# Kernel tuning notes

Hardware: AMD Instinct MI355X
Metric: run time of the kernel (lower is better)

Reference implementation:

```python
import jax, jax.numpy as jnp
import numpy as np

B, S, D, H, MB = 2, 2048, 2048, 32, 16
HD = D // H          # 64
N = S // MB          # 128 mini-batches
EPS = 1e-5
BASE_LR = 1.0


def setup_inputs() -> dict:
    ks = jax.random.split(jax.random.key(0), 8)
    sc = 1.0 / np.sqrt(D)
    inv = 1.0 / (10000.0 ** (np.arange(0, HD, 2, dtype=np.float64) / HD))
    return {
        "x": jax.random.normal(ks[0], (B, S, D), jnp.float32),
        "pos_frequencies": jnp.asarray(np.outer(np.arange(S), inv), jnp.float32),  # (S, HD//2) rope angles
        "Wq": jax.random.normal(ks[1], (D, D), jnp.float32) * sc,
        "Wk": jax.random.normal(ks[2], (D, D), jnp.float32) * sc,
        "Wv": jax.random.normal(ks[3], (D, D), jnp.float32) * sc,
        "Wo": jax.random.normal(ks[4], (D, D), jnp.float32) * sc,
        "post_gamma": jnp.ones((D,), jnp.float32),
        "post_beta": jnp.zeros((D,), jnp.float32),
        "ilr_W": jax.random.normal(ks[5], (H, 1, D), jnp.float32) * 0.02,  # inner_loop_lr_W
        "ilr_b": jnp.zeros((H, 1), jnp.float32),                            # inner_loop_lr_b
        "lgs": jnp.zeros((MB,), jnp.float32),                               # learnable_gradient_scale
        "ttt_gamma": jnp.ones((H, HD), jnp.float32),                        # ttt_norm_weight
        "ttt_beta": jnp.zeros((H, HD), jnp.float32),                        # ttt_norm_bias
        "W0": jax.random.normal(ks[6], (H, HD, HD), jnp.float32) / np.sqrt(HD),
        "b0": jnp.zeros((H, 1, HD), jnp.float32),
    }


def _rope(x, freqs):
    # x: (B,H,S,HD), freqs: (S,HD//2); rotate interleaved pairs
    cos = jnp.cos(freqs)[None, None]
    sin = jnp.sin(freqs)[None, None]
    x1, x2 = x[..., 0::2], x[..., 1::2]
    return jnp.stack([x1 * cos - x2 * sin, x1 * sin + x2 * cos], -1).reshape(x.shape)


def _ln_fwd(z, g, b):
    mu = z.mean(-1, keepdims=True)
    var = z.var(-1, keepdims=True)
    return g * (z - mu) * jax.lax.rsqrt(var + EPS) + b


def _ln_l2_bwd(z, tgt, g, b):
    # grad of 0.5*||LN(z) - tgt||^2 w.r.t. z (fused LayerNorm backward)
    mu = z.mean(-1, keepdims=True)
    var = z.var(-1, keepdims=True)
    rstd = jax.lax.rsqrt(var + EPS)
    zh = (z - mu) * rstd
    dy = (g * zh + b) - tgt
    dzh = dy * g
    return (dzh - dzh.mean(-1, keepdims=True) - zh * (dzh * zh).mean(-1, keepdims=True)) * rstd


def reference(x, pos_frequencies, Wq, Wk, Wv, Wo, post_gamma, post_beta,
              ilr_W, ilr_b, lgs, ttt_gamma, ttt_beta, W0, b0):
    # projections (torch Linear: x @ W.T), shape (B,H,S,HD)
    q = (x @ Wq.T).reshape(B, S, H, HD).transpose(0, 2, 1, 3)
    k = (x @ Wk.T).reshape(B, S, H, HD).transpose(0, 2, 1, 3)
    v = (x @ Wv.T).reshape(B, S, H, HD).transpose(0, 2, 1, 3)
    q = _rope(q, pos_frequencies)
    k = _rope(k, pos_frequencies)
    v = _rope(v, pos_frequencies)  # module applies RoPE to V too

    # inner-loop learning rates: (B,H,N,1,MB), gradient_scale: (MB,1)
    xr = x.reshape(B, N, MB, D)
    lr = jnp.einsum('bnkd,hod->bhnko', xr, ilr_W) + ilr_b.reshape(1, H, 1, 1, 1)
    lr = BASE_LR * jax.nn.sigmoid(lr).transpose(0, 1, 2, 4, 3) / HD
    gs = jnp.clip(1.0 / jnp.arange(1, MB + 1, dtype=jnp.float32) + lgs, 0.0)
    eta = gs.reshape(1, 1, 1, MB, 1) * lr  # (B,H,N,MB,MB)

    to_n = lambda t: t.reshape(B, H, N, MB, -1).transpose(2, 0, 1, 3, 4)
    Qn, Kn, Vn = to_n(q), to_n(k), to_n(v)           # (N,B,H,MB,HD)
    En = eta.transpose(2, 0, 1, 3, 4)                # (N,B,H,MB,MB)

    g = ttt_gamma.reshape(1, H, 1, HD)
    be = ttt_beta.reshape(1, H, 1, HD)
    W_init = jnp.broadcast_to(W0[None], (B, H, HD, HD))
    b_init = jnp.broadcast_to(b0[None], (B, H, 1, HD))

    def step(carry, inp):
        W, bb = carry
        XQ, XK, XV, E = inp
        Z = XK @ W + bb
        grad = _ln_l2_bwd(Z, XV - XK, g, be)                 # (B,H,MB,HD)
        Attn = jnp.tril(XQ @ XK.swapaxes(-1, -2))            # causal dual form
        b_bar = bb - jnp.tril(E) @ grad
        Z_bar = XQ @ W - (E * Attn) @ grad + b_bar
        last_eta = E[..., -1, :, None]                       # (B,H,MB,1)
        W_new = W - jnp.swapaxes(last_eta * XK, -1, -2) @ grad
        b_new = bb - jnp.sum(last_eta * grad, axis=-2, keepdims=True)
        return (W_new, b_new), XQ + _ln_fwd(Z_bar, g, be)

    _, ys = jax.lax.scan(step, (W_init, b_init), (Qn, Kn, Vn, En))  # ys: (N,B,H,MB,HD)
    out = ys.transpose(1, 0, 3, 2, 4).reshape(B, S, D)

    mu = out.mean(-1, keepdims=True)
    var = out.var(-1, keepdims=True)
    out = post_gamma * (out - mu) * jax.lax.rsqrt(var + EPS) + post_beta
    return out @ Wo.T
```

## Files before the change

kernel.cpp:

```cpp
#include <hip/hip_runtime.h>
#include <hip/hip_bf16.h>
#include <math.h>

#define BB 2
#define SS 2048
#define DD 2048
#define HH 32
#define HDD 64
#define MBB 16
#define NN 128

typedef unsigned short u16;
typedef short bf16x8_t __attribute__((ext_vector_type(8)));
typedef float f32x4_t __attribute__((ext_vector_type(4)));

__device__ __forceinline__ float b2f(u16 u) { return __uint_as_float(((unsigned)u) << 16); }
__device__ __forceinline__ u16 f2b(float f) {
    unsigned u = __float_as_uint(f);
    return (u16)((u + 0x7FFFu + ((u >> 16) & 1u)) >> 16);
}
__device__ __forceinline__ unsigned pk2(float a, float b) {
    return (unsigned)f2b(a) | ((unsigned)f2b(b) << 16);
}
__device__ __forceinline__ unsigned pk2r(u16 a, u16 b) { return (unsigned)a | ((unsigned)b << 16); }
__device__ __forceinline__ float wsum(float x) {
    x += __shfl_xor(x, 32);
    x += __shfl_xor(x, 16);
    x += __shfl_xor(x, 8);
    x += __shfl_xor(x, 4);
    x += __shfl_xor(x, 2);
    x += __shfl_xor(x, 1);
    return x;
}

typedef __attribute__((address_space(3))) unsigned int lds_u32;
typedef __attribute__((address_space(1))) const unsigned int glb_u32;
__device__ __forceinline__ void async_copy16(const void* g, void* l) {
    __builtin_amdgcn_global_load_lds((glb_u32*)g, (lds_u32*)l, 16, 0, 0);
}


__global__ __launch_bounds__(256) void k_cvt5(const float* __restrict__ x, const float* __restrict__ wq,
                                              const float* __restrict__ wk, const float* __restrict__ wv,
                                              const float* __restrict__ wo, u16* __restrict__ xb,
                                              u16* __restrict__ wqb, u16* __restrict__ wkb,
                                              u16* __restrict__ wvb, u16* __restrict__ wob) {
    int sl = blockIdx.y;
    long e = (long)(blockIdx.x * 256 + threadIdx.x) * 4;
    if (sl == 5) {
        long n = e >> 11;
        int cin = (int)(e & 2047);
        int hd0 = (cin >> 6) * 64 + ((cin & 63) >> 2);
        const float* src = wo + n * 2048 + hd0;
        float f0 = src[0], f1 = src[16], f2 = src[32], f3 = src[48];
        uint2 o;
        o.x = pk2(f0, f1);
        o.y = pk2(f2, f3);
        *(uint2*)(wob + e) = o;
        return;
    }
    const float* s;
    u16* d;
    if (sl == 0) { s = x; d = xb; }
    else if (sl == 1) { s = x + 4194304; d = xb + 4194304; }
    else if (sl == 2) { s = wq; d = wqb; }
    else if (sl == 3) { s = wk; d = wkb; }
    else { s = wv; d = wvb; }
    float4 f = *(const float4*)(s + e);
    uint2 o;
    o.x = pk2(f.x, f.y);
    o.y = pk2(f.z, f.w);
    *(uint2*)(d + e) = o;
}

__global__ void k_trig(const float* __restrict__ pf, float* __restrict__ ct, float* __restrict__ st) {
    int i = blockIdx.x * 256 + threadIdx.x;
    float f = pf[i];
    ct[i] = cosf(f);
    st[i] = sinf(f);
}

__global__ void k_ppg(const float* __restrict__ pg, const float* __restrict__ pb,
                      float* __restrict__ pgp, float* __restrict__ pbp) {
    int i = blockIdx.x * 256 + threadIdx.x;
    int h = i >> 6, o = i & 63;
    int src = h * 64 + (o >> 2) + (o & 3) * 16;
    pgp[i] = pg[src];
    pbp[i] = pb[src];
}

__global__ __launch_bounds__(256) void k_prep(const u16* __restrict__ qb, const u16* __restrict__ kb,
                                              u16* __restrict__ qc, u16* __restrict__ kc) {
    long row = (long)blockIdx.x * 256 + threadIdx.x;
    const u16* src = (blockIdx.y == 0 ? qb : kb) + row * 64;
    u16* dst = (blockIdx.y == 0 ? qc : kc) + row * 64;
    u16 v[64];
#pragma unroll
    for (int i = 0; i < 8; ++i) *(uint4*)&v[i * 8] = *(const uint4*)(src + i * 8);
    u16 o[64];
#pragma unroll
    for (int d = 0; d < 64; ++d) o[(d & 15) * 4 + (d >> 4)] = v[d];
#pragma unroll
    for (int i = 0; i < 8; ++i) *(uint4*)(dst + i * 8) = *(uint4*)&o[i * 8];
}

template <int EPI>
__global__ __launch_bounds__(256) void k_gemm_bt(const u16* __restrict__ A, const u16* __restrict__ B0,
                                                 const u16* __restrict__ B1, const u16* __restrict__ B2,
                                                 void* __restrict__ C0, void* __restrict__ C1,
                                                 void* __restrict__ C2, int M, int Nn, int K,
                                                 const float* __restrict__ ct, const float* __restrict__ st) {
    __shared__ u16 As[128 * 32];
    __shared__ u16 Bs[128 * 32];
    int z = blockIdx.z;
    const u16* Bm = (z == 0) ? B0 : (z == 1) ? B1 : B2;
    void* Cout = (z == 0) ? C0 : (z == 1) ? C1 : C2;
    int tid = threadIdx.x, lane = tid & 63, wv = tid >> 6;
    int m0 = blockIdx.y * 128, n0 = blockIdx.x * 128;
    int wm = wv >> 1, wn = wv & 1;

    f32x4_t acc[4][4];
    f32x4_t zero = {0.f, 0.f, 0.f, 0.f};
#pragma unroll
    for (int a = 0; a < 4; ++a)
#pragma unroll
        for (int b = 0; b < 4; ++b) acc[a][b] = zero;

    int mrow = lane & 15, qk = (lane >> 4) * 8;
    const int kTiles = K >> 5;
    for (int kt = 0; kt < kTiles; ++kt) {
        __syncthreads();
        int kb = kt << 5;
#pragma unroll
        for (int it = 0; it < 2; ++it) {
            int cb = it * 256 + wv * 64;
            int c = cb + lane;
            const u16* gpA = A + (m0 + (c >> 2)) * K + kb + ((c & 3) << 3);
            async_copy16(gpA, &As[cb << 3]);
            const u16* gpB = Bm + (n0 + (c >> 2)) * K + kb + ((c & 3) << 3);
            async_copy16(gpB, &Bs[cb << 3]);
        }
        asm volatile("s_waitcnt vmcnt(0)" ::: "memory");
        __syncthreads();

        bf16x8_t af[4], bfr[4];
#pragma unroll
        for (int mi = 0; mi < 4; ++mi)
            af[mi] = *(const bf16x8_t*)&As[(wm * 64 + mi * 16 + mrow) * 32 + qk];
#pragma unroll
        for (int ni = 0; ni < 4; ++ni)
            bfr[ni] = *(const bf16x8_t*)&Bs[(wn * 64 + ni * 16 + mrow) * 32 + qk];
#pragma unroll
        for (int mi = 0; mi < 4; ++mi)
#pragma unroll
            for (int ni = 0; ni < 4; ++ni)
                acc[mi][ni] = __builtin_amdgcn_mfma_f32_16x16x32_bf16(af[mi], bfr[ni], acc[mi][ni], 0, 0, 0);
    }

    int col16 = lane & 15, rq = (lane >> 4) * 4;
#pragma unroll
    for (int mi = 0; mi < 4; ++mi) {
#pragma unroll
        for (int ni = 0; ni < 4; ++ni) {
#pragma unroll
            for (int r = 0; r < 4; ++r) {
                int gr = m0 + wm * 64 + mi * 16 + rq + r;
                int gc = n0 + wn * 64 + ni * 16 + col16;
                float val = acc[mi][ni][r];
                if (EPI == 0) {
                    ((float*)Cout)[gr * Nn + gc] = val;
                } else {
                    int b = gr >> 11, s2 = gr & 2047, hh = gc >> 6, hd = gc & 63;
                    int fi = s2 * 32 + (hd >> 1);
                    float c = ct[fi], sn = st[fi];
                    float partner = __shfl_xor(val, 1);
                    float y = (gc & 1) ? (partner * sn + val * c) : (val * c - partner * sn);
                    int po = (z == 2) ? ((hd & 15) * 4 + (hd >> 4)) : hd;
                    ((u16*)Cout)[(((b * HH + hh) * SS) + s2) * HDD + po] = f2b(y);
                }
            }
        }
    }
}

__global__ __launch_bounds__(256) void k_lr(const u16* __restrict__ xb, const float* __restrict__ ilrW,
                                            const float* __restrict__ ilrb, float* __restrict__ lrout) {
    __shared__ u16 xr[4][2048];
    int row0 = blockIdx.x * 4;
    int tid = threadIdx.x, lane = tid & 63, wv = tid >> 6;
    const unsigned* src = (const unsigned*)(xb + row0 * 2048);
    unsigned* dst = (unsigned*)xr;
    for (int i = tid; i < 4096; i += 256) dst[i] = src[i];
    __syncthreads();
    int b = row0 >> 11, s0 = row0 & 2047;
#pragma unroll
    for (int sub = 0; sub < 8; ++sub) {
        int h = wv * 8 + sub;
        const float* wp = ilrW + h * 2048;
        float a0 = 0.f, a1 = 0.f, a2 = 0.f, a3 = 0.f;
        for (int i = 0; i < 16; ++i) {
            int idx = i * 128 + lane * 2;
            float2 w2 = *(const float2*)(wp + idx);
            unsigned p0 = *(const unsigned*)&xr[0][idx];
            unsigned p1 = *(const unsigned*)&xr[1][idx];
            unsigned p2 = *(const unsigned*)&xr[2][idx];
            unsigned p3 = *(const unsigned*)&xr[3][idx];
            a0 += b2f((u16)p0) * w2.x + b2f((u16)(p0 >> 16)) * w2.y;
            a1 += b2f((u16)p1) * w2.x + b2f((u16)(p1 >> 16)) * w2.y;
            a2 += b2f((u16)p2) * w2.x + b2f((u16)(p2 >> 16)) * w2.y;
            a3 += b2f((u16)p3) * w2.x + b2f((u16)(p3 >> 16)) * w2.y;
        }
        a0 = wsum(a0);
        a1 = wsum(a1);
        a2 = wsum(a2);
        a3 = wsum(a3);
        if (lane == 0) {
            float bv = ilrb[h];
            float* op = lrout + ((b * HH + h) * SS) + s0;
            op[0] = (1.0f / (1.0f + expf(-(a0 + bv)))) * (1.0f / 64.0f);
            op[1] = (1.0f / (1.0f + expf(-(a1 + bv)))) * (1.0f / 64.0f);
            op[2] = (1.0f / (1.0f + expf(-(a2 + bv)))) * (1.0f / 64.0f);
            op[3] = (1.0f / (1.0f + expf(-(a3 + bv)))) * (1.0f / 64.0f);
        }
    }
}

__global__ __launch_bounds__(64, 1) void k_scan(const u16* __restrict__ qb, const u16* __restrict__ kb2,
                                                const u16* __restrict__ qc, const u16* __restrict__ kc,
                                                const u16* __restrict__ vc, const float* __restrict__ lrbuf,
                                                const float* __restrict__ lgs, const float* __restrict__ tg,
                                                const float* __restrict__ tb, const float* __restrict__ W0,
                                                const float* __restrict__ b0, u16* __restrict__ ys) {
    __shared__ u16 WbL[64 * 72];
    __shared__ u16 XKT[64 * 40];
    __shared__ u16 GST[64 * 40];
    __shared__ u16 PUL[16 * 40];

    const int bh = blockIdx.x, h = bh & 31, b = bh >> 5;
    const int lane = threadIdx.x & 63;
    const int quad = lane >> 4, col = lane & 15;
    const int base = bh * SS;

    {
        unsigned* p1 = (unsigned*)XKT;
        unsigned* p2 = (unsigned*)GST;
        unsigned* p3 = (unsigned*)PUL;
        for (int i = lane; i < 1280; i += 64) { p1[i] = 0; p2[i] = 0; }
        for (int i = lane; i < 320; i += 64) p3[i] = 0;
    }

    float gd4[4], bd4[4], bbv[4];
#pragma unroll
    for (int tn = 0; tn < 4; ++tn) {
        gd4[tn] = tg[h * 64 + tn * 16 + col];
        bd4[tn] = tb[h * 64 + tn * 16 + col];
        bbv[tn] = b0[h * 64 + tn * 16 + col];
    }
    float gs4[4];
#pragma unroll
    for (int r = 0; r < 4; ++r) {
        int i = quad * 4 + r;
        gs4[r] = fmaxf(1.f / (float)(i + 1) + lgs[i], 0.f);
    }
    const float gs15 = fmaxf(1.f / 16.f + lgs[15], 0.f);

    f32x4_t Wc[4][4];
#pragma unroll
    for (int tm = 0; tm < 4; ++tm)
#pragma unroll
        for (int tn = 0; tn < 4; ++tn)
#pragma unroll
            for (int r = 0; r < 4; ++r)
                Wc[tm][tn][r] = W0[h * 4096 + (tm * 16 + quad * 4 + r) * 64 + tn * 16 + col];

    {
        unsigned* wb32 = (unsigned*)WbL;
#pragma unroll
        for (int tn = 0; tn < 4; ++tn)
#pragma unroll
            for (int tm = 0; tm < 4; ++tm) {
                int a = (tn * 16 + col) * 36 + tm * 8 + quad * 2;
                wb32[a] = pk2(Wc[tm][tn][0], Wc[tm][tn][1]);
                wb32[a + 1] = pk2(Wc[tm][tn][2], Wc[tm][tn][3]);
            }
    }

    bf16x8_t ka[2], qa[2];
    float lr4[4];
    u16 kraw[16], vraw[16], qraw[16];
    {
        const u16* kp = kb2 + (base + col) * 64;
        const u16* qp = qb + (base + col) * 64;
#pragma unroll
        for (int kh = 0; kh < 2; ++kh) {
            ka[kh] = *(const bf16x8_t*)(kp + kh * 32 + quad * 8);
            qa[kh] = *(const bf16x8_t*)(qp + kh * 32 + quad * 8);
        }
#pragma unroll
        for (int r = 0; r < 4; ++r) lr4[r] = lrbuf[base + quad * 4 + r];
#pragma unroll
        for (int r = 0; r < 4; ++r) {
            long ro = (long)(base + quad * 4 + r) * 64 + col * 4;
            ushort4 tk = *(const ushort4*)(kc + ro);
            ushort4 tv = *(const ushort4*)(vc + ro);
            ushort4 tq = *(const ushort4*)(qc + ro);
            kraw[r] = tk.x; kraw[4 + r] = tk.y; kraw[8 + r] = tk.z; kraw[12 + r] = tk.w;
            vraw[r] = tv.x; vraw[4 + r] = tv.y; vraw[8 + r] = tv.z; vraw[12 + r] = tv.w;
            qraw[r] = tq.x; qraw[4 + r] = tq.y; qraw[8 + r] = tq.z; qraw[12 + r] = tq.w;
        }
    }

    bf16x8_t xkf[4], wbf[4][2];
    {
        unsigned* x32 = (unsigned*)XKT;
#pragma unroll
        for (int tn = 0; tn < 4; ++tn) {
            int a = (tn * 16 + col) * 20 + quad * 2;
            x32[a] = pk2r(kraw[tn * 4 + 0], kraw[tn * 4 + 1]);
            x32[a + 1] = pk2r(kraw[tn * 4 + 2], kraw[tn * 4 + 3]);
        }
#pragma unroll
        for (int t = 0; t < 4; ++t)
            xkf[t] = *(const bf16x8_t*)&XKT[(t * 16 + col) * 40 + quad * 8];
#pragma unroll
        for (int tn = 0; tn < 4; ++tn)
#pragma unroll
            for (int kh = 0; kh < 2; ++kh)
                wbf[tn][kh] = *(const bf16x8_t*)&WbL[(tn * 16 + col) * 72 + kh * 32 + quad * 8];
    }

    const f32x4_t zf = {0.f, 0.f, 0.f, 0.f};

    for (int n = 0; n < NN; ++n) {
        const int s0 = n * 16;

        f32x4_t z[4], xqw[4], attn;
#pragma unroll
        for (int tn = 0; tn < 4; ++tn) {
            z[tn] = __builtin_amdgcn_mfma_f32_16x16x32_bf16(ka[1], wbf[tn][1], zf, 0, 0, 0);
            z[tn] = __builtin_amdgcn_mfma_f32_16x16x32_bf16(ka[0], wbf[tn][0], z[tn], 0, 0, 0);
            xqw[tn] = __builtin_amdgcn_mfma_f32_16x16x32_bf16(qa[1], wbf[tn][1], zf, 0, 0, 0);
            xqw[tn] = __builtin_amdgcn_mfma_f32_16x16x32_bf16(qa[0], wbf[tn][0], xqw[tn], 0, 0, 0);
        }
        attn = __builtin_amdgcn_mfma_f32_16x16x32_bf16(qa[1], ka[1], zf, 0, 0, 0);
        attn = __builtin_amdgcn_mfma_f32_16x16x32_bf16(qa[0], ka[0], attn, 0, 0, 0);

#pragma unroll
        for (int r = 0; r < 4; ++r) {
            float pv = (col <= quad * 4 + r) ? (1.f + attn[r]) : 0.f;
            PUL[(quad * 4 + r) * 40 + col] = f2b(pv);
        }

        bf16x8_t nka[2], nqa[2];
        float nlr[4];
        u16 nkraw[16], nvraw[16], nqraw[16];
        {
            const int sp = (n + 1 < NN) ? s0 + 16 : s0;
            const u16* kp = kb2 + (base + sp + col) * 64;
            const u16* qp = qb + (base + sp + col) * 64;
#pragma unroll
            for (int kh = 0; kh < 2; ++kh) {
                nka[kh] = *(const bf16x8_t*)(kp + kh * 32 + quad * 8);
                nqa[kh] = *(const bf16x8_t*)(qp + kh * 32 + quad * 8);
            }
#pragma unroll
            for (int r = 0; r < 4; ++r) nlr[r] = lrbuf[base + sp + quad * 4 + r];
#pragma unroll
            for (int r = 0; r < 4; ++r) {
                long ro = (long)(base + sp + quad * 4 + r) * 64 + col * 4;
                ushort4 tk = *(const ushort4*)(kc + ro);
                ushort4 tv = *(const ushort4*)(vc + ro);
                ushort4 tq = *(const ushort4*)(qc + ro);
                nkraw[r] = tk.x; nkraw[4 + r] = tk.y; nkraw[8 + r] = tk.z; nkraw[12 + r] = tk.w;
                nvraw[r] = tv.x; nvraw[4 + r] = tv.y; nvraw[8 + r] = tv.z; nvraw[12 + r] = tv.w;
                nqraw[r] = tq.x; nqraw[4 + r] = tq.y; nqraw[8 + r] = tq.z; nqraw[12 + r] = tq.w;
            }
        }

#pragma unroll
        for (int tn = 0; tn < 4; ++tn)
#pragma unroll
            for (int r = 0; r < 4; ++r) z[tn][r] += bbv[tn];

        float mu4[4], rstd4[4], m1[4], m2[4];
#pragma unroll
        for (int r = 0; r < 4; ++r) {
            float s1 = z[0][r] + z[1][r] + z[2][r] + z[3][r];
            float s2 = z[0][r] * z[0][r] + z[1][r] * z[1][r] + z[2][r] * z[2][r] + z[3][r] * z[3][r];
#pragma unroll
            for (int m = 1; m <= 8; m <<= 1) { s1 += __shfl_xor(s1, m); s2 += __shfl_xor(s2, m); }
            float mu = s1 * (1.f / 64.f);
            float var = s2 * (1.f / 64.f) - mu * mu;
            mu4[r] = mu;
            rstd4[r] = rsqrtf(var + 1e-5f);
            m1[r] = 0.f;
            m2[r] = 0.f;
        }
#pragma unroll
        for (int tn = 0; tn < 4; ++tn)
#pragma unroll
            for (int r = 0; r < 4; ++r) {
                float zh = (z[tn][r] - mu4[r]) * rstd4[r];
                float tgt = b2f(vraw[tn * 4 + r]) - b2f(kraw[tn * 4 + r]);
                float dzh = (gd4[tn] * zh + bd4[tn] - tgt) * gd4[tn];
                m1[r] += dzh;
                m2[r] += dzh * zh;
            }
#pragma unroll
        for (int r = 0; r < 4; ++r) {
#pragma unroll
            for (int m = 1; m <= 8; m <<= 1) { m1[r] += __shfl_xor(m1[r], m); m2[r] += __shfl_xor(m2[r], m); }
            m1[r] *= (1.f / 64.f);
            m2[r] *= (1.f / 64.f);
        }
        float gS[4][4];
#pragma unroll
        for (int tn = 0; tn < 4; ++tn)
#pragma unroll
            for (int r = 0; r < 4; ++r) {
                float zh = (z[tn][r] - mu4[r]) * rstd4[r];
                float tgt = b2f(vraw[tn * 4 + r]) - b2f(kraw[tn * 4 + r]);
                float dzh = (gd4[tn] * zh + bd4[tn] - tgt) * gd4[tn];
                gS[tn][r] = lr4[r] * ((dzh - m1[r] - zh * m2[r]) * rstd4[r]);
            }
        {
            unsigned* g32 = (unsigned*)GST;
#pragma unroll
            for (int tn = 0; tn < 4; ++tn) {
                int a = (tn * 16 + col) * 20 + quad * 2;
                g32[a] = pk2(gS[tn][0], gS[tn][1]);
                g32[a + 1] = pk2(gS[tn][2], gS[tn][3]);
            }
        }

        bf16x8_t gsf[4], puf;
#pragma unroll
        for (int t = 0; t < 4; ++t)
            gsf[t] = *(const bf16x8_t*)&GST[(t * 16 + col) * 40 + quad * 8];
        puf = *(const bf16x8_t*)&PUL[col * 40 + quad * 8];

#pragma unroll
        for (int tm = 0; tm < 4; ++tm)
#pragma unroll
            for (int tn = 0; tn < 4; ++tn) {
                f32x4_t dw = __builtin_amdgcn_mfma_f32_16x16x32_bf16(xkf[tm], gsf[tn], zf, 0, 0, 0);
#pragma unroll
                for (int r = 0; r < 4; ++r) Wc[tm][tn][r] -= gs15 * dw[r];
            }
        {
            unsigned* wb32 = (unsigned*)WbL;
#pragma unroll
            for (int tn = 0; tn < 4; ++tn)
#pragma unroll
                for (int tm = 0; tm < 4; ++tm) {
                    int a = (tn * 16 + col) * 36 + tm * 8 + quad * 2;
                    wb32[a] = pk2(Wc[tm][tn][0], Wc[tm][tn][1]);
                    wb32[a + 1] = pk2(Wc[tm][tn][2], Wc[tm][tn][3]);
                }
        }

#pragma unroll
        for (int tn = 0; tn < 4; ++tn) {
            f32x4_t pg = __builtin_amdgcn_mfma_f32_16x16x32_bf16(puf, gsf[tn], zf, 0, 0, 0);
#pragma unroll
            for (int r = 0; r < 4; ++r) z[tn][r] = xqw[tn][r] + bbv[tn] - gs4[r] * pg[r];
        }
#pragma unroll
        for (int r = 0; r < 4; ++r) {
            float s1 = z[0][r] + z[1][r] + z[2][r] + z[3][r];
            float s2 = z[0][r] * z[0][r] + z[1][r] * z[1][r] + z[2][r] * z[2][r] + z[3][r] * z[3][r];
#pragma unroll
            for (int m = 1; m <= 8; m <<= 1) { s1 += __shfl_xor(s1, m); s2 += __shfl_xor(s2, m); }
            float mu = s1 * (1.f / 64.f);
            float var = s2 * (1.f / 64.f) - mu * mu;
            mu4[r] = mu;
            rstd4[r] = rsqrtf(var + 1e-5f);
        }
#pragma unroll
        for (int r = 0; r < 4; ++r) {
            ushort4 yv;
            float y0 = b2f(qraw[0 * 4 + r]) + gd4[0] * (z[0][r] - mu4[r]) * rstd4[r] + bd4[0];
            float y1 = b2f(qraw[1 * 4 + r]) + gd4[1] * (z[1][r] - mu4[r]) * rstd4[r] + bd4[1];
            float y2 = b2f(qraw[2 * 4 + r]) + gd4[2] * (z[2][r] - mu4[r]) * rstd4[r] + bd4[2];
            float y3 = b2f(qraw[3 * 4 + r]) + gd4[3] * (z[3][r] - mu4[r]) * rstd4[r] + bd4[3];
            yv.x = f2b(y0); yv.y = f2b(y1); yv.z = f2b(y2); yv.w = f2b(y3);
            *(ushort4*)(ys + (long)(b * SS + s0 + quad * 4 + r) * DD + h * 64 + col * 4) = yv;
        }

#pragma unroll
        for (int tn = 0; tn < 4; ++tn) {
            float c = gS[tn][0] + gS[tn][1] + gS[tn][2] + gS[tn][3];
            c += __shfl_xor(c, 16);
            c += __shfl_xor(c, 32);
            bbv[tn] -= gs15 * c;
        }

        {
            unsigned* x32 = (unsigned*)XKT;
#pragma unroll
            for (int tn = 0; tn < 4; ++tn) {
                int a = (tn * 16 + col) * 20 + quad * 2;
                x32[a] = pk2r(nkraw[tn * 4 + 0], nkraw[tn * 4 + 1]);
                x32[a + 1] = pk2r(nkraw[tn * 4 + 2], nkraw[tn * 4 + 3]);
            }
#pragma unroll
            for (int t = 0; t < 4; ++t)
                xkf[t] = *(const bf16x8_t*)&XKT[(t * 16 + col) * 40 + quad * 8];
#pragma unroll
            for (int tn = 0; tn < 4; ++tn)
#pragma unroll
                for (int kh = 0; kh < 2; ++kh)
                    wbf[tn][kh] = *(const bf16x8_t*)&WbL[(tn * 16 + col) * 72 + kh * 32 + quad * 8];
        }

        ka[0] = nka[0]; ka[1] = nka[1];
        qa[0] = nqa[0]; qa[1] = nqa[1];
#pragma unroll
        for (int r = 0; r < 4; ++r) lr4[r] = nlr[r];
#pragma unroll
        for (int j = 0; j < 16; ++j) { kraw[j] = nkraw[j]; vraw[j] = nvraw[j]; qraw[j] = nqraw[j]; }
    }
}

__global__ __launch_bounds__(256) void k_postln(const u16* __restrict__ ys, const float* __restrict__ pg,
                                                const float* __restrict__ pb, u16* __restrict__ outb) {
    __shared__ float red[8];
    int row = blockIdx.x, tid = threadIdx.x, lane = tid & 63, wv = tid >> 6;
    const u16* rp = ys + row * 2048 + tid * 8;
    uint4 pkd = *(const uint4*)rp;
    float v[8];
    v[0] = b2f((u16)pkd.x); v[1] = b2f((u16)(pkd.x >> 16));
    v[2] = b2f((u16)pkd.y); v[3] = b2f((u16)(pkd.y >> 16));
    v[4] = b2f((u16)pkd.z); v[5] = b2f((u16)(pkd.z >> 16));
    v[6] = b2f((u16)pkd.w); v[7] = b2f((u16)(pkd.w >> 16));
    float s1 = 0.f, s2 = 0.f;
#pragma unroll
    for (int i = 0; i < 8; ++i) { s1 += v[i]; s2 += v[i] * v[i]; }
    s1 = wsum(s1);
    s2 = wsum(s2);
    if (lane == 0) {
        red[wv] = s1;
        red[wv + 4] = s2;
    }
    __syncthreads();
    float S1 = red[0] + red[1] + red[2] + red[3];
    float S2 = red[4] + red[5] + red[6] + red[7];
    float mu = S1 * (1.f / 2048), var = S2 * (1.f / 2048) - mu * mu;
    float rstd = rsqrtf(var + 1e-5f);
    const float4 g0 = *(const float4*)(pg + tid * 8);
    const float4 g1 = *(const float4*)(pg + tid * 8 + 4);
    const float4 b0v = *(const float4*)(pb + tid * 8);
    const float4 b1v = *(const float4*)(pb + tid * 8 + 4);
    float o[8];
    o[0] = g0.x * (v[0] - mu) * rstd + b0v.x;
    o[1] = g0.y * (v[1] - mu) * rstd + b0v.y;
    o[2] = g0.z * (v[2] - mu) * rstd + b0v.z;
    o[3] = g0.w * (v[3] - mu) * rstd + b0v.w;
    o[4] = g1.x * (v[4] - mu) * rstd + b1v.x;
    o[5] = g1.y * (v[5] - mu) * rstd + b1v.y;
    o[6] = g1.z * (v[6] - mu) * rstd + b1v.z;
    o[7] = g1.w * (v[7] - mu) * rstd + b1v.w;
    uint4 po;
    po.x = pk2(o[0], o[1]);
    po.y = pk2(o[2], o[3]);
    po.z = pk2(o[4], o[5]);
    po.w = pk2(o[6], o[7]);
    *(uint4*)(outb + row * 2048 + tid * 8) = po;
}

extern "C" void kernel_launch(void* const* d_in, const int* in_sizes, int n_in,
                              void* d_out, int out_size, void* d_ws, size_t ws_size,
                              hipStream_t stream) {
    const float* x = (const float*)d_in[0];
    const float* pf = (const float*)d_in[1];
    const float* Wq = (const float*)d_in[2];
    const float* Wk = (const float*)d_in[3];
    const float* Wv = (const float*)d_in[4];
    const float* Wo = (const float*)d_in[5];
    const float* pg = (const float*)d_in[6];
    const float* pb = (const float*)d_in[7];
    const float* ilrW = (const float*)d_in[8];
    const float* ilrb = (const float*)d_in[9];
    const float* lgs = (const float*)d_in[10];
    const float* tg = (const float*)d_in[11];
    const float* tb = (const float*)d_in[12];
    const float* W0 = (const float*)d_in[13];
    const float* b0 = (const float*)d_in[14];
    float* out = (float*)d_out;
    char* ws = (char*)d_ws;

    u16* xbf = (u16*)(ws + 0);
    u16* wqb = (u16*)(ws + 16777216);
    u16* wkb = (u16*)(ws + 25165824);
    u16* wvb = (u16*)(ws + 33554432);
    u16* wob = (u16*)(ws + 41943040);
    u16* qbuf = (u16*)(ws + 50331648);
    u16* kbuf = (u16*)(ws + 67108864);
    u16* vbuf = (u16*)(ws + 83886080);
    float* ct = (float*)(ws + 100663296);
    float* st = (float*)(ws + 100925440);
    float* lrb = (float*)(ws + 101187584);
    u16* ysb = (u16*)(ws + 101711872);
    float* pgp = (float*)(ws + 118489088);
    float* pbp = (float*)(ws + 118497280);
    u16* qc = (u16*)(ws + 16777216);
    u16* kc = (u16*)(ws + 0);
    u16* lnb = (u16*)(ws + 0);

    k_cvt5<<<dim3(4096, 6), 256, 0, stream>>>(x, Wq, Wk, Wv, Wo, xbf, wqb, wkb, wvb, wob);
    k_trig<<<256, 256, 0, stream>>>(pf, ct, st);
    k_ppg<<<8, 256, 0, stream>>>(pg, pb, pgp, pbp);

    k_gemm_bt<1><<<dim3(16, 32, 3), 256, 0, stream>>>(xbf, wqb, wkb, wvb, qbuf, kbuf, vbuf,
                                                      4096, 2048, 2048, ct, st);

    k_lr<<<1024, 256, 0, stream>>>(xbf, ilrW, ilrb, lrb);

    k_prep<<<dim3(512, 2), 256, 0, stream>>>(qbuf, kbuf, qc, kc);

    k_scan<<<64, 64, 0, stream>>>(qbuf, kbuf, qc, kc, vbuf, lrb, lgs, tg, tb, W0, b0, ysb);

    k_postln<<<4096, 256, 0, stream>>>(ysb, pgp, pbp, lnb);
    k_gemm_bt<0><<<dim3(16, 32, 1), 256, 0, stream>>>(lnb, wob, wob, wob, out, out, out,
                                                      4096, 2048, 2048, nullptr, nullptr);
}
```

Baseline: 876.3 us.

## Drop k_prep transpose, fuse LN-backward reductions into one pass, use hardware bf16 pack

Removes the k_prep kernel that rearranged Q/K into a column-interleaved copy. The scan now reads the needed elements directly from qbuf/kbuf using strided scalar loads. The LayerNorm backward statistics are rewritten algebraically so that mean, variance and the two gradient reductions are all computed from one set of per-row sums in a single shuffle pass, which shortens the serial dependency chain in each scan step. Software bf16 rounding is replaced with the v_cvt_pk_bf16_f32 instruction. The trade-off is less coalesced global loads in the scan prefetch and possible numerical differences from the expanded moment formulas.

```diff
diff --git a/kernel.cpp b/kernel.cpp
--- a/kernel.cpp
+++ b/kernel.cpp
@@ -21,6 +21,11 @@
 }
 __device__ __forceinline__ unsigned pk2(float a, float b) {
     return (unsigned)f2b(a) | ((unsigned)f2b(b) << 16);
+}
+__device__ __forceinline__ unsigned cvtpk(float lo, float hi) {
+    unsigned r;
+    asm("v_cvt_pk_bf16_f32 %0, %1, %2" : "=v"(r) : "v"(lo), "v"(hi));
+    return r;
 }
 __device__ __forceinline__ unsigned pk2r(u16 a, u16 b) { return (unsigned)a | ((unsigned)b << 16); }
 __device__ __forceinline__ float wsum(float x) {
@@ -89,21 +94,6 @@
     pbp[i] = pb[src];
 }
 
-__global__ __launch_bounds__(256) void k_prep(const u16* __restrict__ qb, const u16* __restrict__ kb,
-                                              u16* __restrict__ qc, u16* __restrict__ kc) {
-    long row = (long)blockIdx.x * 256 + threadIdx.x;
-    const u16* src = (blockIdx.y == 0 ? qb : kb) + row * 64;
-    u16* dst = (blockIdx.y == 0 ? qc : kc) + row * 64;
-    u16 v[64];
-#pragma unroll
-    for (int i = 0; i < 8; ++i) *(uint4*)&v[i * 8] = *(const uint4*)(src + i * 8);
-    u16 o[64];
-#pragma unroll
-    for (int d = 0; d < 64; ++d) o[(d & 15) * 4 + (d >> 4)] = v[d];
-#pragma unroll
-    for (int i = 0; i < 8; ++i) *(uint4*)(dst + i * 8) = *(uint4*)&o[i * 8];
-}
-
 template <int EPI>
 __global__ __launch_bounds__(256) void k_gemm_bt(const u16* __restrict__ A, const u16* __restrict__ B0,
                                                  const u16* __restrict__ B1, const u16* __restrict__ B2,
@@ -226,7 +216,6 @@
 }
 
 __global__ __launch_bounds__(64, 1) void k_scan(const u16* __restrict__ qb, const u16* __restrict__ kb2,
-                                                const u16* __restrict__ qc, const u16* __restrict__ kc,
                                                 const u16* __restrict__ vc, const float* __restrict__ lrbuf,
                                                 const float* __restrict__ lgs, const float* __restrict__ tg,
                                                 const float* __restrict__ tb, const float* __restrict__ W0,
@@ -249,12 +238,21 @@
         for (int i = lane; i < 320; i += 64) p3[i] = 0;
     }
 
-    float gd4[4], bd4[4], bbv[4];
+    float gd4[4], bd4[4], bbv[4], g2[4], gb[4];
 #pragma unroll
     for (int tn = 0; tn < 4; ++tn) {
         gd4[tn] = tg[h * 64 + tn * 16 + col];
         bd4[tn] = tb[h * 64 + tn * 16 + col];
         bbv[tn] = b0[h * 64 + tn * 16 + col];
+        g2[tn] = gd4[tn] * gd4[tn];
+        gb[tn] = gd4[tn] * bd4[tn];
+    }
+    float G2m;
+    {
+        float s = g2[0] + g2[1] + g2[2] + g2[3];
+#pragma unroll
+        for (int m = 1; m <= 8; m <<= 1) s += __shfl_xor(s, m);
+        G2m = s * (1.f / 64.f);
     }
     float gs4[4];
 #pragma unroll
@@ -280,8 +278,8 @@
 #pragma unroll
             for (int tm = 0; tm < 4; ++tm) {
                 int a = (tn * 16 + col) * 36 + tm * 8 + quad * 2;
-                wb32[a] = pk2(Wc[tm][tn][0], Wc[tm][tn][1]);
-                wb32[a + 1] = pk2(Wc[tm][tn][2], Wc[tm][tn][3]);
+                wb32[a] = cvtpk(Wc[tm][tn][0], Wc[tm][tn][1]);
+                wb32[a + 1] = cvtpk(Wc[tm][tn][2], Wc[tm][tn][3]);
             }
     }
 
@@ -299,14 +297,18 @@
 #pragma unroll
         for (int r = 0; r < 4; ++r) lr4[r] = lrbuf[base + quad * 4 + r];
 #pragma unroll
+        for (int tn = 0; tn < 4; ++tn)
+#pragma unroll
+            for (int r = 0; r < 4; ++r) {
+                int idx = (base + quad * 4 + r) * 64 + tn * 16 + col;
+                kraw[tn * 4 + r] = kb2[idx];
+                qraw[tn * 4 + r] = qb[idx];
+            }
+#pragma unroll
         for (int r = 0; r < 4; ++r) {
             long ro = (long)(base + quad * 4 + r) * 64 + col * 4;
-            ushort4 tk = *(const ushort4*)(kc + ro);
             ushort4 tv = *(const ushort4*)(vc + ro);
-            ushort4 tq = *(const ushort4*)(qc + ro);
-            kraw[r] = tk.x; kraw[4 + r] = tk.y; kraw[8 + r] = tk.z; kraw[12 + r] = tk.w;
             vraw[r] = tv.x; vraw[4 + r] = tv.y; vraw[8 + r] = tv.z; vraw[12 + r] = tv.w;
-            qraw[r] = tq.x; qraw[4 + r] = tq.y; qraw[8 + r] = tq.z; qraw[12 + r] = tq.w;
         }
     }
 
@@ -366,14 +368,18 @@
 #pragma unroll
             for (int r = 0; r < 4; ++r) nlr[r] = lrbuf[base + sp + quad * 4 + r];
 #pragma unroll
+            for (int tn = 0; tn < 4; ++tn)
+#pragma unroll
+                for (int r = 0; r < 4; ++r) {
+                    int idx = (base + sp + quad * 4 + r) * 64 + tn * 16 + col;
+                    nkraw[tn * 4 + r] = kb2[idx];
+                    nqraw[tn * 4 + r] = qb[idx];
+                }
+#pragma unroll
             for (int r = 0; r < 4; ++r) {
                 long ro = (long)(base + sp + quad * 4 + r) * 64 + col * 4;
-                ushort4 tk = *(const ushort4*)(kc + ro);
                 ushort4 tv = *(const ushort4*)(vc + ro);
-                ushort4 tq = *(const ushort4*)(qc + ro);
-                nkraw[r] = tk.x; nkraw[4 + r] = tk.y; nkraw[8 + r] = tk.z; nkraw[12 + r] = tk.w;
                 nvraw[r] = tv.x; nvraw[4 + r] = tv.y; nvraw[8 + r] = tv.z; nvraw[12 + r] = tv.w;
-                nqraw[r] = tq.x; nqraw[4 + r] = tq.y; nqraw[8 + r] = tq.z; nqraw[12 + r] = tq.w;
             }
         }
 
@@ -382,7 +388,105 @@
 #pragma unroll
             for (int r = 0; r < 4; ++r) z[tn][r] += bbv[tn];
 
-        float mu4[4], rstd4[4], m1[4], m2[4];
+        float c1[16];
+        float A1[4], A2[4], A3[4], A4[4], A5[4], A6[4];
+#pragma unroll
+        for (int r = 0; r < 4; ++r) { A1[r] = 0.f; A2[r] = 0.f; A3[r] = 0.f; A4[r] = 0.f; A5[r] = 0.f; A6[r] = 0.f; }
+#pragma unroll
+        for (int tn = 0; tn < 4; ++tn)
+#pragma unroll
+            for (int r = 0; r < 4; ++r) {
+                float zv = z[tn][r];
+                float tgt = b2f(vraw[tn * 4 + r]) - b2f(kraw[tn * 4 + r]);
+                float c = gb[tn] - gd4[tn] * tgt;
+                c1[tn * 4 + r] = c;
+                float t = g2[tn] * zv;
+                A1[r] += zv;
+                A2[r] = fmaf(zv, zv, A2[r]);
+                A3[r] += t;
+                A4[r] = fmaf(t, zv, A4[r]);
+                A5[r] = fmaf(c, zv, A5[r]);
+                A6[r] += c;
+            }
+#pragma unroll
+        for (int m = 1; m <= 8; m <<= 1) {
+#pragma unroll
+            for (int r = 0; r < 4; ++r) {
+                A1[r] += __shfl_xor(A1[r], m);
+                A2[r] += __shfl_xor(A2[r], m);
+                A3[r] += __shfl_xor(A3[r], m);
+                A4[r] += __shfl_xor(A4[r], m);
+                A5[r] += __shfl_xor(A5[r], m);
+                A6[r] += __shfl_xor(A6[r], m);
+            }
+        }
+        float mu4[4], rstd4[4], m1[4], m2[4], rl[4];
+#pragma unroll
+        for (int r = 0; r < 4; ++r) {
+            float mu = A1[r] * (1.f / 64.f);
+            float var = A2[r] * (1.f / 64.f) - mu * mu;
+            float rstd = rsqrtf(var + 1e-5f);
+            float T1m = A3[r] * (1.f / 64.f);
+            float T2m = A4[r] * (1.f / 64.f);
+            float T3m = A5[r] * (1.f / 64.f);
+            float C1m = A6[r] * (1.f / 64.f);
+            m1[r] = rstd * (T1m - mu * G2m) + C1m;
+            m2[r] = rstd * rstd * (T2m - 2.f * mu * T1m + mu * mu * G2m) + rstd * (T3m - mu * C1m);
+            mu4[r] = mu;
+            rstd4[r] = rstd;
+            rl[r] = rstd * lr4[r];
+        }
+        float gS[4][4];
+#pragma unroll
+        for (int tn = 0; tn < 4; ++tn)
+#pragma unroll
+            for (int r = 0; r < 4; ++r) {
+                float zh = (z[tn][r] - mu4[r]) * rstd4[r];
+                float dzh = fmaf(g2[tn], zh, c1[tn * 4 + r]);
+                gS[tn][r] = fmaf(-m2[r], zh, dzh - m1[r]) * rl[r];
+            }
+        {
+            unsigned* g32 = (unsigned*)GST;
+#pragma unroll
+            for (int tn = 0; tn < 4; ++tn) {
+                int a = (tn * 16 + col) * 20 + quad * 2;
+                g32[a] = cvtpk(gS[tn][0], gS[tn][1]);
+                g32[a + 1] = cvtpk(gS[tn][2], gS[tn][3]);
+            }
+        }
+
+        bf16x8_t gsf[4], puf;
+#pragma unroll
+        for (int t = 0; t < 4; ++t)
+            gsf[t] = *(const bf16x8_t*)&GST[(t * 16 + col) * 40 + quad * 8];
+        puf = *(const bf16x8_t*)&PUL[col * 40 + quad * 8];
+
+#pragma unroll
+        for (int tm = 0; tm < 4; ++tm)
+#pragma unroll
+            for (int tn = 0; tn < 4; ++tn) {
+                f32x4_t dw = __builtin_amdgcn_mfma_f32_16x16x32_bf16(xkf[tm], gsf[tn], zf, 0, 0, 0);
+#pragma unroll
+                for (int r = 0; r < 4; ++r) Wc[tm][tn][r] -= gs15 * dw[r];
+            }
+        {
+            unsigned* wb32 = (unsigned*)WbL;
+#pragma unroll
+            for (int tn = 0; tn < 4; ++tn)
+#pragma unroll
+                for (int tm = 0; tm < 4; ++tm) {
+                    int a = (tn * 16 + col) * 36 + tm * 8 + quad * 2;
+                    wb32[a] = cvtpk(Wc[tm][tn][0], Wc[tm][tn][1]);
+                    wb32[a + 1] = cvtpk(Wc[tm][tn][2], Wc[tm][tn][3]);
+                }
+        }
+
+#pragma unroll
+        for (int tn = 0; tn < 4; ++tn) {
+            f32x4_t pg = __builtin_amdgcn_mfma_f32_16x16x32_bf16(puf, gsf[tn], zf, 0, 0, 0);
+#pragma unroll
+            for (int r = 0; r < 4; ++r) z[tn][r] = xqw[tn][r] + bbv[tn] - gs4[r] * pg[r];
+        }
 #pragma unroll
         for (int r = 0; r < 4; ++r) {
             float s1 = z[0][r] + z[1][r] + z[2][r] + z[3][r];
@@ -393,98 +497,17 @@
             float var = s2 * (1.f / 64.f) - mu * mu;
             mu4[r] = mu;
             rstd4[r] = rsqrtf(var + 1e-5f);
-            m1[r] = 0.f;
-            m2[r] = 0.f;
-        }
-#pragma unroll
-        for (int tn = 0; tn < 4; ++tn)
-#pragma unroll
-            for (int r = 0; r < 4; ++r) {
-                float zh = (z[tn][r] - mu4[r]) * rstd4[r];
-                float tgt = b2f(vraw[tn * 4 + r]) - b2f(kraw[tn * 4 + r]);
-                float dzh = (gd4[tn] * zh + bd4[tn] - tgt) * gd4[tn];
-                m1[r] += dzh;
-                m2[r] += dzh * zh;
-            }
+        }
 #pragma unroll
         for (int r = 0; r < 4; ++r) {
-#pragma unroll
-            for (int m = 1; m <= 8; m <<= 1) { m1[r] += __shfl_xor(m1[r], m); m2[r] += __shfl_xor(m2[r], m); }
-            m1[r] *= (1.f / 64.f);
-            m2[r] *= (1.f / 64.f);
-        }
-        float gS[4][4];
-#pragma unroll
-        for (int tn = 0; tn < 4; ++tn)
-#pragma unroll
-            for (int r = 0; r < 4; ++r) {
-                float zh = (z[tn][r] - mu4[r]) * rstd4[r];
-                float tgt = b2f(vraw[tn * 4 + r]) - b2f(kraw[tn * 4 + r]);
-                float dzh = (gd4[tn] * zh + bd4[tn] - tgt) * gd4[tn];
-                gS[tn][r] = lr4[r] * ((dzh - m1[r] - zh * m2[r]) * rstd4[r]);
-            }
-        {
-            unsigned* g32 = (unsigned*)GST;
-#pragma unroll
-            for (int tn = 0; tn < 4; ++tn) {
-                int a = (tn * 16 + col) * 20 + quad * 2;
-                g32[a] = pk2(gS[tn][0], gS[tn][1]);
-                g32[a + 1] = pk2(gS[tn][2], gS[tn][3]);
-            }
-        }
-
-        bf16x8_t gsf[4], puf;
-#pragma unroll
-        for (int t = 0; t < 4; ++t)
-            gsf[t] = *(const bf16x8_t*)&GST[(t * 16 + col) * 40 + quad * 8];
-        puf = *(const bf16x8_t*)&PUL[col * 40 + quad * 8];
-
-#pragma unroll
-        for (int tm = 0; tm < 4; ++tm)
-#pragma unroll
-            for (int tn = 0; tn < 4; ++tn) {
-                f32x4_t dw = __builtin_amdgcn_mfma_f32_16x16x32_bf16(xkf[tm], gsf[tn], zf, 0, 0, 0);
-#pragma unroll
-                for (int r = 0; r < 4; ++r) Wc[tm][tn][r] -= gs15 * dw[r];
-            }
-        {
-            unsigned* wb32 = (unsigned*)WbL;
-#pragma unroll
-            for (int tn = 0; tn < 4; ++tn)
-#pragma unroll
-                for (int tm = 0; tm < 4; ++tm) {
-                    int a = (tn * 16 + col) * 36 + tm * 8 + quad * 2;
-                    wb32[a] = pk2(Wc[tm][tn][0], Wc[tm][tn][1]);
-                    wb32[a + 1] = pk2(Wc[tm][tn][2], Wc[tm][tn][3]);
-                }
-        }
-
-#pragma unroll
-        for (int tn = 0; tn < 4; ++tn) {
-            f32x4_t pg = __builtin_amdgcn_mfma_f32_16x16x32_bf16(puf, gsf[tn], zf, 0, 0, 0);
-#pragma unroll
-            for (int r = 0; r < 4; ++r) z[tn][r] = xqw[tn][r] + bbv[tn] - gs4[r] * pg[r];
-        }
-#pragma unroll
-        for (int r = 0; r < 4; ++r) {
-            float s1 = z[0][r] + z[1][r] + z[2][r] + z[3][r];
-            float s2 = z[0][r] * z[0][r] + z[1][r] * z[1][r] + z[2][r] * z[2][r] + z[3][r] * z[3][r];
-#pragma unroll
-            for (int m = 1; m <= 8; m <<= 1) { s1 += __shfl_xor(s1, m); s2 += __shfl_xor(s2, m); }
-            float mu = s1 * (1.f / 64.f);
-            float var = s2 * (1.f / 64.f) - mu * mu;
-            mu4[r] = mu;
-            rstd4[r] = rsqrtf(var + 1e-5f);
-        }
-#pragma unroll
-        for (int r = 0; r < 4; ++r) {
-            ushort4 yv;
             float y0 = b2f(qraw[0 * 4 + r]) + gd4[0] * (z[0][r] - mu4[r]) * rstd4[r] + bd4[0];
             float y1 = b2f(qraw[1 * 4 + r]) + gd4[1] * (z[1][r] - mu4[r]) * rstd4[r] + bd4[1];
             float y2 = b2f(qraw[2 * 4 + r]) + gd4[2] * (z[2][r] - mu4[r]) * rstd4[r] + bd4[2];
             float y3 = b2f(qraw[3 * 4 + r]) + gd4[3] * (z[3][r] - mu4[r]) * rstd4[r] + bd4[3];
-            yv.x = f2b(y0); yv.y = f2b(y1); yv.z = f2b(y2); yv.w = f2b(y3);
-            *(ushort4*)(ys + (long)(b * SS + s0 + quad * 4 + r) * DD + h * 64 + col * 4) = yv;
+            uint2 po;
+            po.x = cvtpk(y0, y1);
+            po.y = cvtpk(y2, y3);
+            *(uint2*)(ys + (long)(b * SS + s0 + quad * 4 + r) * DD + h * 64 + col * 4) = po;
         }
 
 #pragma unroll
@@ -603,8 +626,6 @@
     u16* ysb = (u16*)(ws + 101711872);
     float* pgp = (float*)(ws + 118489088);
     float* pbp = (float*)(ws + 118497280);
-    u16* qc = (u16*)(ws + 16777216);
-    u16* kc = (u16*)(ws + 0);
     u16* lnb = (u16*)(ws + 0);
 
     k_cvt5<<<dim3(4096, 6), 256, 0, stream>>>(x, Wq, Wk, Wv, Wo, xbf, wqb, wkb, wvb, wob);
@@ -616,9 +637,7 @@
 
     k_lr<<<1024, 256, 0, stream>>>(xbf, ilrW, ilrb, lrb);
 
-    k_prep<<<dim3(512, 2), 256, 0, stream>>>(qbuf, kbuf, qc, kc);
-
-    k_scan<<<64, 64, 0, stream>>>(qbuf, kbuf, qc, kc, vbuf, lrb, lgs, tg, tb, W0, b0, ysb);
+    k_scan<<<64, 64, 0, stream>>>(qbuf, kbuf, vbuf, lrb, lgs, tg, tb, W0, b0, ysb);
 
     k_postln<<<4096, 256, 0, stream>>>(ysb, pgp, pbp, lnb);
     k_gemm_bt<0><<<dim3(16, 32, 1), 256, 0, stream>>>(lnb, wob, wob, wob, out, out, out,
```

New measurement: 798.6 us. -8.9%, faster.
